# Performance work log

Measured on AMD Instinct MI355X. Metric: run time of the kernel, lower is better.

The kernel has to match this reference:

```python
import jax, jax.numpy as jnp
import numpy as np

G, N, D, E, L, OUT = 64, 1024, 128, 16384, 2, 64


def setup_inputs() -> dict:
    key = jax.random.key(0)
    ks = jax.random.split(key, 7)
    input_feature = jax.random.normal(ks[0], (G, N, D), jnp.float32)
    edge_index = jax.random.randint(ks[1], (G, 2, E), 0, N, jnp.int32)
    # GraphConv(D, 1): lin_rel (with bias) applied to aggregated neighbors, lin_root (no bias)
    w_rel = jax.random.normal(ks[2], (L, D), jnp.float32) / np.sqrt(D).astype(np.float32)
    b_rel = jnp.zeros((L,), jnp.float32)
    w_root = jax.random.normal(ks[3], (L, D), jnp.float32) / np.sqrt(D).astype(np.float32)
    # SelectTopK(1, ratio): weight is a [1,1] scalar per layer
    w_sel = jax.random.normal(ks[4], (L,), jnp.float32) + 1.5  # keep away from 0
    W_lin = jax.random.normal(ks[5], (2 * D, OUT), jnp.float32) / np.sqrt(2 * D).astype(np.float32)
    b_lin = jnp.zeros((OUT,), jnp.float32)
    return dict(input_feature=input_feature, edge_index=edge_index, w_rel=w_rel,
                b_rel=b_rel, w_root=w_root, w_sel=w_sel, W_lin=W_lin, b_lin=b_lin)


def _sagpool(x, ei, emask, w_rel, b_rel, w_root, w_sel):
    # x: [g, n, d]; ei: [g, 2, e]; emask: [g, e] bool (invalid edges contribute zero)
    g, n, d = x.shape
    src, dst = ei[:, 0], ei[:, 1]  # [g, e] (source_to_target flow)
    gidx = jnp.arange(g)[:, None]
    # GraphConv attention score (out_channels = 1)
    msg = jnp.take_along_axis(x, src[..., None], axis=1) * emask[..., None].astype(x.dtype)  # [g,e,d]
    agg = jnp.zeros_like(x).at[gidx, dst].add(msg)  # segment-sum over dst, [g,n,d]
    attn = agg @ w_rel + b_rel + x @ w_root  # [g, n]
    # SelectTopK: score = tanh(attn * w / ||w||), then per-graph top-k (k = n//2 since ratio=0.5)
    score = jnp.tanh(attn * (w_sel / jnp.abs(w_sel)))
    k = n // 2
    top_s, perm = jax.lax.top_k(score, k)  # [g, k]
    new_x = jnp.take_along_axis(x, perm[..., None], axis=1) * top_s[..., None]  # [g, k, d]
    # FilterEdges: keep edges with both endpoints selected, remap to new node ids
    new_idx = jnp.full((g, n), -1, jnp.int32).at[gidx, perm].set(
        jnp.broadcast_to(jnp.arange(k, dtype=jnp.int32)[None, :], (g, k)))
    src2 = jnp.take_along_axis(new_idx, src, axis=1)
    dst2 = jnp.take_along_axis(new_idx, dst, axis=1)
    new_mask = emask & (src2 >= 0) & (dst2 >= 0)
    src2 = jnp.where(new_mask, src2, 0)
    dst2 = jnp.where(new_mask, dst2, 0)
    return new_x, jnp.stack([src2, dst2], axis=1), new_mask


def reference(input_feature, edge_index, w_rel, b_rel, w_root, w_sel, W_lin, b_lin):
    x, ei = input_feature, edge_index
    emask = jnp.ones((ei.shape[0], ei.shape[2]), dtype=bool)
    for l in range(L):
        x, ei, emask = _sagpool(x, ei, emask, w_rel[l], b_rel[l], w_root[l], w_sel[l])
    # global_mean_pool || global_max_pool per graph, then Linear(2D -> OUT)
    readout = jnp.concatenate([x.mean(axis=1), x.max(axis=1)], axis=-1)  # [G, 2D]
    return readout @ W_lin + b_lin
```

## Files before the change

kernel.cpp:

```cpp
#include <hip/hip_runtime.h>
#include <stdint.h>

#define NG   64
#define N0   1024
#define N1   512
#define K2   256
#define DD   128
#define NE   16384
#define NOUT 64

__device__ __forceinline__ float waveReduceSum(float v) {
    for (int off = 32; off > 0; off >>= 1) v += __shfl_xor(v, off, 64);
    return v;
}

template<int NN>
__device__ __forceinline__ unsigned long long bitonic_desc(
    unsigned long long key, unsigned long long* lds, int i)
{
    for (int k2 = 2; k2 <= NN; k2 <<= 1) {
        for (int j = k2 >> 1; j > 0; j >>= 1) {
            unsigned long long p;
            if (j >= 64) {
                __syncthreads();
                lds[i] = key;
                __syncthreads();
                p = lds[i ^ j];
            } else {
                p = __shfl_xor(key, j, 64);
            }
            bool keepMax = (((i & k2) == 0) == ((i & j) == 0));
            if (keepMax ? (p > key) : (p < key)) key = p;
        }
    }
    return key;
}

__device__ __forceinline__ unsigned long long make_key(float attnv, float sgn, int i, int nn) {
    float sc = tanhf(attnv * sgn);
    unsigned int u = __float_as_uint(sc);
    u = (u & 0x80000000u) ? ~u : (u | 0x80000000u);
    return ((unsigned long long)u << 32) | (unsigned int)(nn - 1 - i);
}

__global__ __launch_bounds__(256) void dots1_kernel(
    const float* __restrict__ x,
    const float* __restrict__ w_rel, const float* __restrict__ w_root,
    const float* __restrict__ b_rel_p,
    float* __restrict__ s_rel, float* __restrict__ attn,
    int totalNodes)
{
    int wave = blockIdx.x * 4 + (threadIdx.x >> 6);
    int lane = threadIdx.x & 63;
    float wr0 = w_rel[lane * 2],  wr1 = w_rel[lane * 2 + 1];
    float wo0 = w_root[lane * 2], wo1 = w_root[lane * 2 + 1];
    float brel = *b_rel_p;
    #pragma unroll
    for (int t = 0; t < 4; ++t) {
        int node = wave * 4 + t;
        if (node >= totalNodes) return;
        const float2 v = *(const float2*)(x + (size_t)node * DD + lane * 2);
        float pr = waveReduceSum(v.x * wr0 + v.y * wr1);
        float po = waveReduceSum(v.x * wo0 + v.y * wo1);
        if (lane == 0) { s_rel[node] = pr; attn[node] = po + brel; }
    }
}

__global__ __launch_bounds__(1024) void graph1_kernel(
    const float* __restrict__ s_rel1,
    const float* __restrict__ attn1in,
    const float* __restrict__ w_sel_p,
    const int*   __restrict__ ei,
    int*   __restrict__ perm1,
    float* __restrict__ tops1,
    int*   __restrict__ newidx1)
{
    __shared__ float srel[N0];
    __shared__ float attn[N0];
    __shared__ unsigned long long keys[N0];
    const int g = blockIdx.x, i = threadIdx.x;

    srel[i] = s_rel1[(size_t)g * N0 + i];
    attn[i] = attn1in[(size_t)g * N0 + i];
    __syncthreads();

    const int* base = ei + (size_t)g * 2 * NE;
    #pragma unroll
    for (int it = 0; it < 4; ++it) {
        int eo = (it * 1024 + i) * 4;
        const int4 s4 = *(const int4*)(base + eo);
        const int4 d4 = *(const int4*)(base + NE + eo);
        atomicAdd(&attn[d4.x], srel[s4.x]);
        atomicAdd(&attn[d4.y], srel[s4.y]);
        atomicAdd(&attn[d4.z], srel[s4.z]);
        atomicAdd(&attn[d4.w], srel[s4.w]);
    }
    __syncthreads();

    const float sgn = (*w_sel_p >= 0.f) ? 1.f : -1.f;
    unsigned long long key = make_key(attn[i], sgn, i, N0);
    key = bitonic_desc<N0>(key, keys, i);

    int idx = (N0 - 1) - (int)(key & 0xffffffffu);
    unsigned int ku = (unsigned int)(key >> 32);
    unsigned int fb = (ku & 0x80000000u) ? (ku ^ 0x80000000u) : ~ku;
    if (i < N1) {
        perm1[(size_t)g * N1 + i] = idx;
        tops1[(size_t)g * N1 + i] = __uint_as_float(fb);
    }
    newidx1[(size_t)g * N0 + idx] = (i < N1) ? i : -1;
}

__global__ __launch_bounds__(256) void gdots2_kernel(
    const float* __restrict__ x0,
    const int*   __restrict__ perm1,
    const float* __restrict__ tops1,
    const float* __restrict__ w_rel, const float* __restrict__ w_root,
    const float* __restrict__ b_rel_p,
    float* __restrict__ s_rel2, float* __restrict__ attn2,
    int totalOut)
{
    int wave = blockIdx.x * 4 + (threadIdx.x >> 6);
    int lane = threadIdx.x & 63;
    float wr0 = w_rel[lane * 2],  wr1 = w_rel[lane * 2 + 1];
    float wo0 = w_root[lane * 2], wo1 = w_root[lane * 2 + 1];
    float brel = *b_rel_p;
    #pragma unroll
    for (int t = 0; t < 4; ++t) {
        int j = wave * 4 + t;
        if (j >= totalOut) return;
        int g = j >> 9;
        int node = perm1[j];
        float scl = tops1[j];
        const float2 v = *(const float2*)(x0 + ((size_t)(g << 10) + node) * DD + lane * 2);
        float pr = waveReduceSum(v.x * wr0 + v.y * wr1);
        float po = waveReduceSum(v.x * wo0 + v.y * wo1);
        if (lane == 0) { s_rel2[j] = scl * pr; attn2[j] = scl * po + brel; }
    }
}

__global__ __launch_bounds__(512) void graph2_readout_kernel(
    const float* __restrict__ x0,
    const int*   __restrict__ ei,
    const int*   __restrict__ newidx1,
    const int*   __restrict__ perm1,
    const float* __restrict__ tops1,
    const float* __restrict__ s_rel2,
    const float* __restrict__ attn2in,
    const float* __restrict__ w_sel_p,
    const float* __restrict__ W_lin,
    const float* __restrict__ b_lin,
    float* __restrict__ out)
{
    __shared__ int   nidx[N0];
    __shared__ float srel[N1];
    __shared__ float attn[N1];
    __shared__ unsigned long long keys[N1];
    __shared__ int   p1l[N1];
    __shared__ float t1l[N1];
    __shared__ int   cn0[K2];
    __shared__ float cs[K2];
    __shared__ float sm[4][DD], mm[4][DD], rr[2 * DD], po[4][NOUT];

    const int g = blockIdx.x, i = threadIdx.x;
    nidx[i]       = newidx1[(size_t)g * N0 + i];
    nidx[i + 512] = newidx1[(size_t)g * N0 + i + 512];
    srel[i] = s_rel2[(size_t)g * N1 + i];
    attn[i] = attn2in[(size_t)g * N1 + i];
    p1l[i]  = perm1[(size_t)g * N1 + i];
    t1l[i]  = tops1[(size_t)g * N1 + i];
    __syncthreads();

    const int* base = ei + (size_t)g * 2 * NE;
    #pragma unroll
    for (int it = 0; it < 8; ++it) {
        int eo = (it * 512 + i) * 4;
        const int4 s4 = *(const int4*)(base + eo);
        const int4 d4 = *(const int4*)(base + NE + eo);
        int s2, d2;
        s2 = nidx[s4.x]; d2 = nidx[d4.x]; if ((s2 | d2) >= 0) atomicAdd(&attn[d2], srel[s2]);
        s2 = nidx[s4.y]; d2 = nidx[d4.y]; if ((s2 | d2) >= 0) atomicAdd(&attn[d2], srel[s2]);
        s2 = nidx[s4.z]; d2 = nidx[d4.z]; if ((s2 | d2) >= 0) atomicAdd(&attn[d2], srel[s2]);
        s2 = nidx[s4.w]; d2 = nidx[d4.w]; if ((s2 | d2) >= 0) atomicAdd(&attn[d2], srel[s2]);
    }
    __syncthreads();

    const float sgn = (*w_sel_p >= 0.f) ? 1.f : -1.f;
    unsigned long long key = make_key(attn[i], sgn, i, N1);
    key = bitonic_desc<N1>(key, keys, i);

    int idx = (N1 - 1) - (int)(key & 0xffffffffu);
    unsigned int ku = (unsigned int)(key >> 32);
    unsigned int fb = (ku & 0x80000000u) ? (ku ^ 0x80000000u) : ~ku;
    if (i < K2) {
        cn0[i] = p1l[idx];
        cs[i]  = __uint_as_float(fb) * t1l[idx];
    }
    __syncthreads();

    const int d = i & (DD - 1), q = i >> 7;
    float sum = 0.f, mx = -3.0e38f;
    #pragma unroll 4
    for (int j = q * 64; j < q * 64 + 64; ++j) {
        float v = x0[((size_t)(g << 10) + cn0[j]) * DD + d] * cs[j];
        sum += v;
        mx = fmaxf(mx, v);
    }
    sm[q][d] = sum; mm[q][d] = mx;
    __syncthreads();
    if (i < DD) {
        rr[i] = (sm[0][i] + sm[1][i] + sm[2][i] + sm[3][i]) * (1.f / 256.f);
    } else if (i < 2 * DD) {
        int dd = i - DD;
        rr[DD + dd] = fmaxf(fmaxf(mm[0][dd], mm[1][dd]), fmaxf(mm[2][dd], mm[3][dd]));
    }
    __syncthreads();
    if (i < 256) {
        int o = i & (NOUT - 1), c = i >> 6;
        float acc = 0.f;
        #pragma unroll
        for (int i2 = 0; i2 < 64; ++i2) {
            int ii = c * 64 + i2;
            acc += rr[ii] * W_lin[ii * NOUT + o];
        }
        po[c][o] = acc;
    }
    __syncthreads();
    if (i < NOUT)
        out[(size_t)g * NOUT + i] =
            b_lin[i] + po[0][i] + po[1][i] + po[2][i] + po[3][i];
}

extern "C" void kernel_launch(void* const* d_in, const int* in_sizes, int n_in,
                              void* d_out, int out_size, void* d_ws, size_t ws_size,
                              hipStream_t stream)
{
    const float* x0     = (const float*)d_in[0];
    const int*   ei     = (const int*)  d_in[1];
    const float* w_rel  = (const float*)d_in[2];
    const float* b_rel  = (const float*)d_in[3];
    const float* w_root = (const float*)d_in[4];
    const float* w_sel  = (const float*)d_in[5];
    const float* W_lin  = (const float*)d_in[6];
    const float* b_lin  = (const float*)d_in[7];
    float* out = (float*)d_out;
    (void)in_sizes; (void)n_in; (void)out_size; (void)ws_size;

    char* ws = (char*)d_ws;
    size_t off = 0;
    auto alloc = [&](size_t bytes) -> void* {
        off = (off + 255) & ~(size_t)255;
        void* p = ws + off;
        off += bytes;
        return p;
    };

    float* s_rel1  = (float*)alloc((size_t)NG * N0 * 4);
    float* attn1   = (float*)alloc((size_t)NG * N0 * 4);
    int*   perm1   = (int*)  alloc((size_t)NG * N1 * 4);
    float* tops1   = (float*)alloc((size_t)NG * N1 * 4);
    int*   newidx1 = (int*)  alloc((size_t)NG * N0 * 4);
    float* s_rel2  = (float*)alloc((size_t)NG * N1 * 4);
    float* attn2   = (float*)alloc((size_t)NG * N1 * 4);

    dots1_kernel<<<(NG * N0) / 16, 256, 0, stream>>>(
        x0, w_rel, w_root, b_rel, s_rel1, attn1, NG * N0);

    graph1_kernel<<<NG, 1024, 0, stream>>>(
        s_rel1, attn1, w_sel, ei, perm1, tops1, newidx1);

    gdots2_kernel<<<(NG * N1) / 16, 256, 0, stream>>>(
        x0, perm1, tops1, w_rel + DD, w_root + DD, b_rel + 1,
        s_rel2, attn2, NG * N1);

    graph2_readout_kernel<<<NG, 512, 0, stream>>>(
        x0, ei, newidx1, perm1, tops1, s_rel2, attn2, w_sel + 1,
        W_lin, b_lin, out);
}
```

Baseline: 162.3 us.

## Fuse all four SAGPool stages into one per-graph kernel

```diff
diff --git a/kernel.cpp b/kernel.cpp
--- a/kernel.cpp
+++ b/kernel.cpp
@@ -43,48 +43,53 @@
     return ((unsigned long long)u << 32) | (unsigned int)(nn - 1 - i);
 }
 
-__global__ __launch_bounds__(256) void dots1_kernel(
-    const float* __restrict__ x,
-    const float* __restrict__ w_rel, const float* __restrict__ w_root,
-    const float* __restrict__ b_rel_p,
-    float* __restrict__ s_rel, float* __restrict__ attn,
-    int totalNodes)
-{
-    int wave = blockIdx.x * 4 + (threadIdx.x >> 6);
-    int lane = threadIdx.x & 63;
-    float wr0 = w_rel[lane * 2],  wr1 = w_rel[lane * 2 + 1];
-    float wo0 = w_root[lane * 2], wo1 = w_root[lane * 2 + 1];
-    float brel = *b_rel_p;
-    #pragma unroll
-    for (int t = 0; t < 4; ++t) {
-        int node = wave * 4 + t;
-        if (node >= totalNodes) return;
-        const float2 v = *(const float2*)(x + (size_t)node * DD + lane * 2);
-        float pr = waveReduceSum(v.x * wr0 + v.y * wr1);
-        float po = waveReduceSum(v.x * wo0 + v.y * wo1);
-        if (lane == 0) { s_rel[node] = pr; attn[node] = po + brel; }
-    }
-}
-
-__global__ __launch_bounds__(1024) void graph1_kernel(
-    const float* __restrict__ s_rel1,
-    const float* __restrict__ attn1in,
-    const float* __restrict__ w_sel_p,
+__global__ __launch_bounds__(1024) void sag_all_kernel(
+    const float* __restrict__ x0,
     const int*   __restrict__ ei,
-    int*   __restrict__ perm1,
-    float* __restrict__ tops1,
-    int*   __restrict__ newidx1)
+    const float* __restrict__ w_rel,
+    const float* __restrict__ b_rel,
+    const float* __restrict__ w_root,
+    const float* __restrict__ w_sel,
+    const float* __restrict__ W_lin,
+    const float* __restrict__ b_lin,
+    float* __restrict__ out)
 {
     __shared__ float srel[N0];
     __shared__ float attn[N0];
     __shared__ unsigned long long keys[N0];
+    __shared__ int   nidx[N0];
+    __shared__ int   p1l[N1];
+    __shared__ float t1l[N1];
+    __shared__ float srel2[N1];
+    __shared__ float attn2[N1];
+    __shared__ int   cn0[K2];
+    __shared__ float cs[K2];
+    __shared__ float sm[4][DD], mm[4][DD], rr[2 * DD], po[4][NOUT];
+
     const int g = blockIdx.x, i = threadIdx.x;
-
-    srel[i] = s_rel1[(size_t)g * N0 + i];
-    attn[i] = attn1in[(size_t)g * N0 + i];
-    __syncthreads();
-
-    const int* base = ei + (size_t)g * 2 * NE;
+    const int wave = i >> 6, lane = i & 63;
+    const float* xg   = x0 + (size_t)g * N0 * DD;
+    const int*   base = ei + (size_t)g * 2 * NE;
+
+    {
+        float wr0 = w_rel[lane * 2],  wr1 = w_rel[lane * 2 + 1];
+        float wo0 = w_root[lane * 2], wo1 = w_root[lane * 2 + 1];
+        float brel = b_rel[0];
+        #pragma unroll
+        for (int it = 0; it < 16; ++it) {
+            int rowBase = (it * 16 + wave) * 4;
+            #pragma unroll
+            for (int t = 0; t < 4; ++t) {
+                int row = rowBase + t;
+                const float2 v = *(const float2*)(xg + (size_t)row * DD + lane * 2);
+                float pr  = waveReduceSum(v.x * wr0 + v.y * wr1);
+                float po_ = waveReduceSum(v.x * wo0 + v.y * wo1);
+                if (lane == 0) { srel[row] = pr; attn[row] = po_ + brel; }
+            }
+        }
+    }
+    __syncthreads();
+
     #pragma unroll
     for (int it = 0; it < 4; ++it) {
         int eo = (it * 1024 + i) * 4;
@@ -97,116 +102,77 @@
     }
     __syncthreads();
 
-    const float sgn = (*w_sel_p >= 0.f) ? 1.f : -1.f;
-    unsigned long long key = make_key(attn[i], sgn, i, N0);
-    key = bitonic_desc<N0>(key, keys, i);
-
-    int idx = (N0 - 1) - (int)(key & 0xffffffffu);
-    unsigned int ku = (unsigned int)(key >> 32);
-    unsigned int fb = (ku & 0x80000000u) ? (ku ^ 0x80000000u) : ~ku;
-    if (i < N1) {
-        perm1[(size_t)g * N1 + i] = idx;
-        tops1[(size_t)g * N1 + i] = __uint_as_float(fb);
-    }
-    newidx1[(size_t)g * N0 + idx] = (i < N1) ? i : -1;
-}
-
-__global__ __launch_bounds__(256) void gdots2_kernel(
-    const float* __restrict__ x0,
-    const int*   __restrict__ perm1,
-    const float* __restrict__ tops1,
-    const float* __restrict__ w_rel, const float* __restrict__ w_root,
-    const float* __restrict__ b_rel_p,
-    float* __restrict__ s_rel2, float* __restrict__ attn2,
-    int totalOut)
-{
-    int wave = blockIdx.x * 4 + (threadIdx.x >> 6);
-    int lane = threadIdx.x & 63;
-    float wr0 = w_rel[lane * 2],  wr1 = w_rel[lane * 2 + 1];
-    float wo0 = w_root[lane * 2], wo1 = w_root[lane * 2 + 1];
-    float brel = *b_rel_p;
+    {
+        const float sgn = (w_sel[0] >= 0.f) ? 1.f : -1.f;
+        unsigned long long key = make_key(attn[i], sgn, i, N0);
+        key = bitonic_desc<N0>(key, keys, i);
+        int idx = (N0 - 1) - (int)(key & 0xffffffffu);
+        unsigned int ku = (unsigned int)(key >> 32);
+        unsigned int fb = (ku & 0x80000000u) ? (ku ^ 0x80000000u) : ~ku;
+        nidx[idx] = (i < N1) ? i : -1;
+        if (i < N1) { p1l[i] = idx; t1l[i] = __uint_as_float(fb); }
+    }
+    __syncthreads();
+
+    {
+        float wr0 = w_rel[DD + lane * 2],  wr1 = w_rel[DD + lane * 2 + 1];
+        float wo0 = w_root[DD + lane * 2], wo1 = w_root[DD + lane * 2 + 1];
+        float brel = b_rel[1];
+        #pragma unroll
+        for (int it = 0; it < 8; ++it) {
+            int jBase = (it * 16 + wave) * 4;
+            #pragma unroll
+            for (int t = 0; t < 4; ++t) {
+                int j = jBase + t;
+                int node = p1l[j];
+                float scl = t1l[j];
+                const float2 v = *(const float2*)(xg + (size_t)node * DD + lane * 2);
+                float pr  = waveReduceSum(v.x * wr0 + v.y * wr1);
+                float po_ = waveReduceSum(v.x * wo0 + v.y * wo1);
+                if (lane == 0) { srel2[j] = scl * pr; attn2[j] = scl * po_ + brel; }
+            }
+        }
+    }
+    __syncthreads();
+
     #pragma unroll
-    for (int t = 0; t < 4; ++t) {
-        int j = wave * 4 + t;
-        if (j >= totalOut) return;
-        int g = j >> 9;
-        int node = perm1[j];
-        float scl = tops1[j];
-        const float2 v = *(const float2*)(x0 + ((size_t)(g << 10) + node) * DD + lane * 2);
-        float pr = waveReduceSum(v.x * wr0 + v.y * wr1);
-        float po = waveReduceSum(v.x * wo0 + v.y * wo1);
-        if (lane == 0) { s_rel2[j] = scl * pr; attn2[j] = scl * po + brel; }
-    }
-}
-
-__global__ __launch_bounds__(512) void graph2_readout_kernel(
-    const float* __restrict__ x0,
-    const int*   __restrict__ ei,
-    const int*   __restrict__ newidx1,
-    const int*   __restrict__ perm1,
-    const float* __restrict__ tops1,
-    const float* __restrict__ s_rel2,
-    const float* __restrict__ attn2in,
-    const float* __restrict__ w_sel_p,
-    const float* __restrict__ W_lin,
-    const float* __restrict__ b_lin,
-    float* __restrict__ out)
-{
-    __shared__ int   nidx[N0];
-    __shared__ float srel[N1];
-    __shared__ float attn[N1];
-    __shared__ unsigned long long keys[N1];
-    __shared__ int   p1l[N1];
-    __shared__ float t1l[N1];
-    __shared__ int   cn0[K2];
-    __shared__ float cs[K2];
-    __shared__ float sm[4][DD], mm[4][DD], rr[2 * DD], po[4][NOUT];
-
-    const int g = blockIdx.x, i = threadIdx.x;
-    nidx[i]       = newidx1[(size_t)g * N0 + i];
-    nidx[i + 512] = newidx1[(size_t)g * N0 + i + 512];
-    srel[i] = s_rel2[(size_t)g * N1 + i];
-    attn[i] = attn2in[(size_t)g * N1 + i];
-    p1l[i]  = perm1[(size_t)g * N1 + i];
-    t1l[i]  = tops1[(size_t)g * N1 + i];
-    __syncthreads();
-
-    const int* base = ei + (size_t)g * 2 * NE;
-    #pragma unroll
-    for (int it = 0; it < 8; ++it) {
-        int eo = (it * 512 + i) * 4;
+    for (int it = 0; it < 4; ++it) {
+        int eo = (it * 1024 + i) * 4;
         const int4 s4 = *(const int4*)(base + eo);
         const int4 d4 = *(const int4*)(base + NE + eo);
         int s2, d2;
-        s2 = nidx[s4.x]; d2 = nidx[d4.x]; if ((s2 | d2) >= 0) atomicAdd(&attn[d2], srel[s2]);
-        s2 = nidx[s4.y]; d2 = nidx[d4.y]; if ((s2 | d2) >= 0) atomicAdd(&attn[d2], srel[s2]);
-        s2 = nidx[s4.z]; d2 = nidx[d4.z]; if ((s2 | d2) >= 0) atomicAdd(&attn[d2], srel[s2]);
-        s2 = nidx[s4.w]; d2 = nidx[d4.w]; if ((s2 | d2) >= 0) atomicAdd(&attn[d2], srel[s2]);
-    }
-    __syncthreads();
-
-    const float sgn = (*w_sel_p >= 0.f) ? 1.f : -1.f;
-    unsigned long long key = make_key(attn[i], sgn, i, N1);
-    key = bitonic_desc<N1>(key, keys, i);
-
-    int idx = (N1 - 1) - (int)(key & 0xffffffffu);
-    unsigned int ku = (unsigned int)(key >> 32);
-    unsigned int fb = (ku & 0x80000000u) ? (ku ^ 0x80000000u) : ~ku;
-    if (i < K2) {
-        cn0[i] = p1l[idx];
-        cs[i]  = __uint_as_float(fb) * t1l[idx];
-    }
-    __syncthreads();
-
-    const int d = i & (DD - 1), q = i >> 7;
-    float sum = 0.f, mx = -3.0e38f;
-    #pragma unroll 4
-    for (int j = q * 64; j < q * 64 + 64; ++j) {
-        float v = x0[((size_t)(g << 10) + cn0[j]) * DD + d] * cs[j];
-        sum += v;
-        mx = fmaxf(mx, v);
-    }
-    sm[q][d] = sum; mm[q][d] = mx;
+        s2 = nidx[s4.x]; d2 = nidx[d4.x]; if ((s2 | d2) >= 0) atomicAdd(&attn2[d2], srel2[s2]);
+        s2 = nidx[s4.y]; d2 = nidx[d4.y]; if ((s2 | d2) >= 0) atomicAdd(&attn2[d2], srel2[s2]);
+        s2 = nidx[s4.z]; d2 = nidx[d4.z]; if ((s2 | d2) >= 0) atomicAdd(&attn2[d2], srel2[s2]);
+        s2 = nidx[s4.w]; d2 = nidx[d4.w]; if ((s2 | d2) >= 0) atomicAdd(&attn2[d2], srel2[s2]);
+    }
+    __syncthreads();
+
+    {
+        const float sgn = (w_sel[1] >= 0.f) ? 1.f : -1.f;
+        unsigned long long key = (i < N1) ? make_key(attn2[i], sgn, i, N1) : 0ULL;
+        key = bitonic_desc<N0>(key, keys, i);
+        if (i < K2) {
+            int idx = (N1 - 1) - (int)(key & 0xffffffffu);
+            unsigned int ku = (unsigned int)(key >> 32);
+            unsigned int fb = (ku & 0x80000000u) ? (ku ^ 0x80000000u) : ~ku;
+            cn0[i] = p1l[idx];
+            cs[i]  = __uint_as_float(fb) * t1l[idx];
+        }
+    }
+    __syncthreads();
+
+    if (i < 512) {
+        const int d = i & (DD - 1), q = i >> 7;
+        float sum = 0.f, mx = -3.0e38f;
+        #pragma unroll 4
+        for (int j = q * 64; j < q * 64 + 64; ++j) {
+            float v = xg[(size_t)cn0[j] * DD + d] * cs[j];
+            sum += v;
+            mx = fmaxf(mx, v);
+        }
+        sm[q][d] = sum; mm[q][d] = mx;
+    }
     __syncthreads();
     if (i < DD) {
         rr[i] = (sm[0][i] + sm[1][i] + sm[2][i] + sm[3][i]) * (1.f / 256.f);
@@ -244,36 +210,8 @@
     const float* W_lin  = (const float*)d_in[6];
     const float* b_lin  = (const float*)d_in[7];
     float* out = (float*)d_out;
-    (void)in_sizes; (void)n_in; (void)out_size; (void)ws_size;
-
-    char* ws = (char*)d_ws;
-    size_t off = 0;
-    auto alloc = [&](size_t bytes) -> void* {
-        off = (off + 255) & ~(size_t)255;
-        void* p = ws + off;
-        off += bytes;
-        return p;
-    };
-
-    float* s_rel1  = (float*)alloc((size_t)NG * N0 * 4);
-    float* attn1   = (float*)alloc((size_t)NG * N0 * 4);
-    int*   perm1   = (int*)  alloc((size_t)NG * N1 * 4);
-    float* tops1   = (float*)alloc((size_t)NG * N1 * 4);
-    int*   newidx1 = (int*)  alloc((size_t)NG * N0 * 4);
-    float* s_rel2  = (float*)alloc((size_t)NG * N1 * 4);
-    float* attn2   = (float*)alloc((size_t)NG * N1 * 4);
-
-    dots1_kernel<<<(NG * N0) / 16, 256, 0, stream>>>(
-        x0, w_rel, w_root, b_rel, s_rel1, attn1, NG * N0);
-
-    graph1_kernel<<<NG, 1024, 0, stream>>>(
-        s_rel1, attn1, w_sel, ei, perm1, tops1, newidx1);
-
-    gdots2_kernel<<<(NG * N1) / 16, 256, 0, stream>>>(
-        x0, perm1, tops1, w_rel + DD, w_root + DD, b_rel + 1,
-        s_rel2, attn2, NG * N1);
-
-    graph2_readout_kernel<<<NG, 512, 0, stream>>>(
-        x0, ei, newidx1, perm1, tops1, s_rel2, attn2, w_sel + 1,
-        W_lin, b_lin, out);
-}
+    (void)in_sizes; (void)n_in; (void)out_size; (void)d_ws; (void)ws_size;
+
+    sag_all_kernel<<<NG, 1024, 0, stream>>>(
+        x0, ei, w_rel, b_rel, w_root, w_sel, W_lin, b_lin, out);
+}
```

Result: slower. 201.7 us (+24.3%).

## Precompute layer-2 projections on all nodes and drop the gather-dot kernel

Applied to the files above, without the earlier changes.

```diff
diff --git a/kernel.cpp b/kernel.cpp
--- a/kernel.cpp
+++ b/kernel.cpp
@@ -43,37 +43,52 @@
     return ((unsigned long long)u << 32) | (unsigned int)(nn - 1 - i);
 }
 
-__global__ __launch_bounds__(256) void dots1_kernel(
+__global__ __launch_bounds__(256) void dots_all_kernel(
     const float* __restrict__ x,
     const float* __restrict__ w_rel, const float* __restrict__ w_root,
-    const float* __restrict__ b_rel_p,
-    float* __restrict__ s_rel, float* __restrict__ attn,
+    const float* __restrict__ b_rel,
+    float* __restrict__ s_rel1, float* __restrict__ attn1,
+    float* __restrict__ s_rel2f, float* __restrict__ s_root2f,
     int totalNodes)
 {
     int wave = blockIdx.x * 4 + (threadIdx.x >> 6);
     int lane = threadIdx.x & 63;
-    float wr0 = w_rel[lane * 2],  wr1 = w_rel[lane * 2 + 1];
-    float wo0 = w_root[lane * 2], wo1 = w_root[lane * 2 + 1];
-    float brel = *b_rel_p;
+    float wr10 = w_rel[lane * 2],       wr11 = w_rel[lane * 2 + 1];
+    float wo10 = w_root[lane * 2],      wo11 = w_root[lane * 2 + 1];
+    float wr20 = w_rel[DD + lane * 2],  wr21 = w_rel[DD + lane * 2 + 1];
+    float wo20 = w_root[DD + lane * 2], wo21 = w_root[DD + lane * 2 + 1];
+    float b0 = b_rel[0];
     #pragma unroll
     for (int t = 0; t < 4; ++t) {
         int node = wave * 4 + t;
         if (node >= totalNodes) return;
         const float2 v = *(const float2*)(x + (size_t)node * DD + lane * 2);
-        float pr = waveReduceSum(v.x * wr0 + v.y * wr1);
-        float po = waveReduceSum(v.x * wo0 + v.y * wo1);
-        if (lane == 0) { s_rel[node] = pr; attn[node] = po + brel; }
+        float p1 = waveReduceSum(v.x * wr10 + v.y * wr11);
+        float p2 = waveReduceSum(v.x * wo10 + v.y * wo11);
+        float p3 = waveReduceSum(v.x * wr20 + v.y * wr21);
+        float p4 = waveReduceSum(v.x * wo20 + v.y * wo21);
+        if (lane == 0) {
+            s_rel1[node]   = p1;
+            attn1[node]    = p2 + b0;
+            s_rel2f[node]  = p3;
+            s_root2f[node] = p4;
+        }
     }
 }
 
 __global__ __launch_bounds__(1024) void graph1_kernel(
     const float* __restrict__ s_rel1,
     const float* __restrict__ attn1in,
-    const float* __restrict__ w_sel_p,
+    const float* __restrict__ s_rel2f,
+    const float* __restrict__ s_root2f,
+    const float* __restrict__ b_rel,
+    const float* __restrict__ w_sel,
     const int*   __restrict__ ei,
     int*   __restrict__ perm1,
     float* __restrict__ tops1,
-    int*   __restrict__ newidx1)
+    int*   __restrict__ newidx1,
+    float* __restrict__ srel2out,
+    float* __restrict__ attn2out)
 {
     __shared__ float srel[N0];
     __shared__ float attn[N0];
@@ -85,69 +100,50 @@
     __syncthreads();
 
     const int* base = ei + (size_t)g * 2 * NE;
-    #pragma unroll
-    for (int it = 0; it < 4; ++it) {
-        int eo = (it * 1024 + i) * 4;
-        const int4 s4 = *(const int4*)(base + eo);
-        const int4 d4 = *(const int4*)(base + NE + eo);
-        atomicAdd(&attn[d4.x], srel[s4.x]);
-        atomicAdd(&attn[d4.y], srel[s4.y]);
-        atomicAdd(&attn[d4.z], srel[s4.z]);
-        atomicAdd(&attn[d4.w], srel[s4.w]);
-    }
-    __syncthreads();
-
-    const float sgn = (*w_sel_p >= 0.f) ? 1.f : -1.f;
+    {
+        int4 s4[4], d4[4];
+        #pragma unroll
+        for (int it = 0; it < 4; ++it) {
+            int eo = (it * 1024 + i) * 4;
+            s4[it] = *(const int4*)(base + eo);
+            d4[it] = *(const int4*)(base + NE + eo);
+        }
+        #pragma unroll
+        for (int it = 0; it < 4; ++it) {
+            atomicAdd(&attn[d4[it].x], srel[s4[it].x]);
+            atomicAdd(&attn[d4[it].y], srel[s4[it].y]);
+            atomicAdd(&attn[d4[it].z], srel[s4[it].z]);
+            atomicAdd(&attn[d4[it].w], srel[s4[it].w]);
+        }
+    }
+    __syncthreads();
+
+    const float sgn = (w_sel[0] >= 0.f) ? 1.f : -1.f;
     unsigned long long key = make_key(attn[i], sgn, i, N0);
     key = bitonic_desc<N0>(key, keys, i);
 
     int idx = (N0 - 1) - (int)(key & 0xffffffffu);
     unsigned int ku = (unsigned int)(key >> 32);
     unsigned int fb = (ku & 0x80000000u) ? (ku ^ 0x80000000u) : ~ku;
+    newidx1[(size_t)g * N0 + idx] = (i < N1) ? i : -1;
     if (i < N1) {
+        float t = __uint_as_float(fb);
         perm1[(size_t)g * N1 + i] = idx;
-        tops1[(size_t)g * N1 + i] = __uint_as_float(fb);
-    }
-    newidx1[(size_t)g * N0 + idx] = (i < N1) ? i : -1;
-}
-
-__global__ __launch_bounds__(256) void gdots2_kernel(
-    const float* __restrict__ x0,
-    const int*   __restrict__ perm1,
-    const float* __restrict__ tops1,
-    const float* __restrict__ w_rel, const float* __restrict__ w_root,
-    const float* __restrict__ b_rel_p,
-    float* __restrict__ s_rel2, float* __restrict__ attn2,
-    int totalOut)
-{
-    int wave = blockIdx.x * 4 + (threadIdx.x >> 6);
-    int lane = threadIdx.x & 63;
-    float wr0 = w_rel[lane * 2],  wr1 = w_rel[lane * 2 + 1];
-    float wo0 = w_root[lane * 2], wo1 = w_root[lane * 2 + 1];
-    float brel = *b_rel_p;
-    #pragma unroll
-    for (int t = 0; t < 4; ++t) {
-        int j = wave * 4 + t;
-        if (j >= totalOut) return;
-        int g = j >> 9;
-        int node = perm1[j];
-        float scl = tops1[j];
-        const float2 v = *(const float2*)(x0 + ((size_t)(g << 10) + node) * DD + lane * 2);
-        float pr = waveReduceSum(v.x * wr0 + v.y * wr1);
-        float po = waveReduceSum(v.x * wo0 + v.y * wo1);
-        if (lane == 0) { s_rel2[j] = scl * pr; attn2[j] = scl * po + brel; }
-    }
-}
-
-__global__ __launch_bounds__(512) void graph2_readout_kernel(
+        tops1[(size_t)g * N1 + i] = t;
+        srel2out[(size_t)g * N1 + i] = t * s_rel2f[(size_t)g * N0 + idx];
+        attn2out[(size_t)g * N1 + i] = t * s_root2f[(size_t)g * N0 + idx] + b_rel[1];
+    }
+}
+
+__global__ __launch_bounds__(1024) void graph2_readout_kernel(
     const float* __restrict__ x0,
     const int*   __restrict__ ei,
     const int*   __restrict__ newidx1,
     const int*   __restrict__ perm1,
     const float* __restrict__ tops1,
-    const float* __restrict__ s_rel2,
+    const float* __restrict__ srel2in,
     const float* __restrict__ attn2in,
-    const float* __restrict__ w_sel_p,
+    const float* __restrict__ w_sel,
     const float* __restrict__ W_lin,
     const float* __restrict__ b_lin,
     float* __restrict__ out)
@@ -155,7 +151,7 @@
     __shared__ int   nidx[N0];
     __shared__ float srel[N1];
     __shared__ float attn[N1];
-    __shared__ unsigned long long keys[N1];
+    __shared__ unsigned long long keys[N0];
     __shared__ int   p1l[N1];
     __shared__ float t1l[N1];
     __shared__ int   cn0[K2];
@@ -163,50 +159,61 @@
     __shared__ float sm[4][DD], mm[4][DD], rr[2 * DD], po[4][NOUT];
 
     const int g = blockIdx.x, i = threadIdx.x;
-    nidx[i]       = newidx1[(size_t)g * N0 + i];
-    nidx[i + 512] = newidx1[(size_t)g * N0 + i + 512];
-    srel[i] = s_rel2[(size_t)g * N1 + i];
-    attn[i] = attn2in[(size_t)g * N1 + i];
-    p1l[i]  = perm1[(size_t)g * N1 + i];
-    t1l[i]  = tops1[(size_t)g * N1 + i];
+    const float* xg = x0 + (size_t)g * N0 * DD;
+    nidx[i] = newidx1[(size_t)g * N0 + i];
+    if (i < N1) {
+        srel[i] = srel2in[(size_t)g * N1 + i];
+        attn[i] = attn2in[(size_t)g * N1 + i];
+        p1l[i]  = perm1[(size_t)g * N1 + i];
+        t1l[i]  = tops1[(size_t)g * N1 + i];
+    }
     __syncthreads();
 
     const int* base = ei + (size_t)g * 2 * NE;
-    #pragma unroll
-    for (int it = 0; it < 8; ++it) {
-        int eo = (it * 512 + i) * 4;
-        const int4 s4 = *(const int4*)(base + eo);
-        const int4 d4 = *(const int4*)(base + NE + eo);
-        int s2, d2;
-        s2 = nidx[s4.x]; d2 = nidx[d4.x]; if ((s2 | d2) >= 0) atomicAdd(&attn[d2], srel[s2]);
-        s2 = nidx[s4.y]; d2 = nidx[d4.y]; if ((s2 | d2) >= 0) atomicAdd(&attn[d2], srel[s2]);
-        s2 = nidx[s4.z]; d2 = nidx[d4.z]; if ((s2 | d2) >= 0) atomicAdd(&attn[d2], srel[s2]);
-        s2 = nidx[s4.w]; d2 = nidx[d4.w]; if ((s2 | d2) >= 0) atomicAdd(&attn[d2], srel[s2]);
-    }
-    __syncthreads();
-
-    const float sgn = (*w_sel_p >= 0.f) ? 1.f : -1.f;
-    unsigned long long key = make_key(attn[i], sgn, i, N1);
-    key = bitonic_desc<N1>(key, keys, i);
-
-    int idx = (N1 - 1) - (int)(key & 0xffffffffu);
-    unsigned int ku = (unsigned int)(key >> 32);
-    unsigned int fb = (ku & 0x80000000u) ? (ku ^ 0x80000000u) : ~ku;
-    if (i < K2) {
-        cn0[i] = p1l[idx];
-        cs[i]  = __uint_as_float(fb) * t1l[idx];
-    }
-    __syncthreads();
-
-    const int d = i & (DD - 1), q = i >> 7;
-    float sum = 0.f, mx = -3.0e38f;
-    #pragma unroll 4
-    for (int j = q * 64; j < q * 64 + 64; ++j) {
-        float v = x0[((size_t)(g << 10) + cn0[j]) * DD + d] * cs[j];
-        sum += v;
-        mx = fmaxf(mx, v);
-    }
-    sm[q][d] = sum; mm[q][d] = mx;
+    {
+        int4 s4[4], d4[4];
+        #pragma unroll
+        for (int it = 0; it < 4; ++it) {
+            int eo = (it * 1024 + i) * 4;
+            s4[it] = *(const int4*)(base + eo);
+            d4[it] = *(const int4*)(base + NE + eo);
+        }
+        #pragma unroll
+        for (int it = 0; it < 4; ++it) {
+            int s2, d2;
+            s2 = nidx[s4[it].x]; d2 = nidx[d4[it].x]; if ((s2 | d2) >= 0) atomicAdd(&attn[d2], srel[s2]);
+            s2 = nidx[s4[it].y]; d2 = nidx[d4[it].y]; if ((s2 | d2) >= 0) atomicAdd(&attn[d2], srel[s2]);
+            s2 = nidx[s4[it].z]; d2 = nidx[d4[it].z]; if ((s2 | d2) >= 0) atomicAdd(&attn[d2], srel[s2]);
+            s2 = nidx[s4[it].w]; d2 = nidx[d4[it].w]; if ((s2 | d2) >= 0) atomicAdd(&attn[d2], srel[s2]);
+        }
+    }
+    __syncthreads();
+
+    {
+        const float sgn = (w_sel[1] >= 0.f) ? 1.f : -1.f;
+        unsigned long long key = (i < N1) ? make_key(attn[i], sgn, i, N1) : 0ULL;
+        key = bitonic_desc<N0>(key, keys, i);
+        if (i < K2) {
+            int idx = (N1 - 1) - (int)(key & 0xffffffffu);
+            unsigned int ku = (unsigned int)(key >> 32);
+            unsigned int fb = (ku & 0x80000000u) ? (ku ^ 0x80000000u) : ~ku;
+            cn0[i] = p1l[idx];
+            cs[i]  = __uint_as_float(fb) * t1l[idx];
+        }
+    }
+    __syncthreads();
+
+    if (i < 512) {
+        const int d = i & (DD - 1), q = i >> 7;
+        float sum = 0.f, mx = -3.0e38f;
+        #pragma unroll 4
+        for (int j = q * 64; j < q * 64 + 64; ++j) {
+            float v = xg[(size_t)cn0[j] * DD + d] * cs[j];
+            sum += v;
+            mx = fmaxf(mx, v);
+        }
+        sm[q][d] = sum; mm[q][d] = mx;
+    }
     __syncthreads();
     if (i < DD) {
         rr[i] = (sm[0][i] + sm[1][i] + sm[2][i] + sm[3][i]) * (1.f / 256.f);
@@ -255,25 +262,24 @@
         return p;
     };
 
-    float* s_rel1  = (float*)alloc((size_t)NG * N0 * 4);
-    float* attn1   = (float*)alloc((size_t)NG * N0 * 4);
-    int*   perm1   = (int*)  alloc((size_t)NG * N1 * 4);
-    float* tops1   = (float*)alloc((size_t)NG * N1 * 4);
-    int*   newidx1 = (int*)  alloc((size_t)NG * N0 * 4);
-    float* s_rel2  = (float*)alloc((size_t)NG * N1 * 4);
-    float* attn2   = (float*)alloc((size_t)NG * N1 * 4);
-
-    dots1_kernel<<<(NG * N0) / 16, 256, 0, stream>>>(
-        x0, w_rel, w_root, b_rel, s_rel1, attn1, NG * N0);
+    float* s_rel1   = (float*)alloc((size_t)NG * N0 * 4);
+    float* attn1    = (float*)alloc((size_t)NG * N0 * 4);
+    float* s_rel2f  = (float*)alloc((size_t)NG * N0 * 4);
+    float* s_root2f = (float*)alloc((size_t)NG * N0 * 4);
+    int*   perm1    = (int*)  alloc((size_t)NG * N1 * 4);
+    float* tops1    = (float*)alloc((size_t)NG * N1 * 4);
+    int*   newidx1  = (int*)  alloc((size_t)NG * N0 * 4);
+    float* srel2    = (float*)alloc((size_t)NG * N1 * 4);
+    float* attn2    = (float*)alloc((size_t)NG * N1 * 4);
+
+    dots_all_kernel<<<(NG * N0) / 16, 256, 0, stream>>>(
+        x0, w_rel, w_root, b_rel, s_rel1, attn1, s_rel2f, s_root2f, NG * N0);
 
     graph1_kernel<<<NG, 1024, 0, stream>>>(
-        s_rel1, attn1, w_sel, ei, perm1, tops1, newidx1);
-
-    gdots2_kernel<<<(NG * N1) / 16, 256, 0, stream>>>(
-        x0, perm1, tops1, w_rel + DD, w_root + DD, b_rel + 1,
-        s_rel2, attn2, NG * N1);
-
-    graph2_readout_kernel<<<NG, 512, 0, stream>>>(
-        x0, ei, newidx1, perm1, tops1, s_rel2, attn2, w_sel + 1,
+        s_rel1, attn1, s_rel2f, s_root2f, b_rel, w_sel, ei,
+        perm1, tops1, newidx1, srel2, attn2);
+
+    graph2_readout_kernel<<<NG, 1024, 0, stream>>>(
+        x0, ei, newidx1, perm1, tops1, srel2, attn2, w_sel + 0,
         W_lin, b_lin, out);
 }
```

Result: slower. 167.2 us (+3.0%).
